# Optimization experiments

Measured on AMD Instinct MI355X. Metric: run time of the kernel, lower is better.

## Reference

```python
import jax, jax.numpy as jnp
import numpy as np

N_NODES = 100000


def gcn_conv(x, edge_index, W, b, n_nodes):
    # h = X W  (transform first, aggregate in the smaller hidden dim)
    h = x @ W
    src, dst = edge_index[0], edge_index[1]
    # add self-loops (GCNConv default, fill_value=1)
    loop = jnp.arange(n_nodes, dtype=src.dtype)
    src = jnp.concatenate([src, loop])
    dst = jnp.concatenate([dst, loop])
    w = jnp.ones(src.shape[0], dtype=x.dtype)
    # symmetric degree normalization: deg^{-1/2}[src] * w * deg^{-1/2}[dst]
    deg = jax.ops.segment_sum(w, dst, num_segments=n_nodes)
    dinv = jnp.where(deg > 0, jax.lax.rsqrt(deg), 0.0).astype(x.dtype)
    norm = dinv[src] * w * dinv[dst]
    # gather messages from src, scale, scatter-add into dst
    out = jax.ops.segment_sum(h[src] * norm[:, None], dst, num_segments=n_nodes)
    return out + b


def setup_inputs() -> dict:
    key = jax.random.key(0)
    k1, k2, k3, k4 = jax.random.split(key, 4)
    n, f, hid, c, e = N_NODES, 512, 64, 40, 1600000
    x = jax.random.normal(k1, (n, f), dtype=jnp.float32)
    edge_index = jax.random.randint(k2, (2, e), 0, n, dtype=jnp.int64)
    W1 = jax.random.normal(k3, (f, hid), dtype=jnp.float32) * (1.0 / np.sqrt(f))
    b1 = jnp.zeros((hid,), dtype=jnp.float32)
    W2 = jax.random.normal(k4, (hid, c), dtype=jnp.float32) * (1.0 / np.sqrt(hid))
    b2 = jnp.zeros((c,), dtype=jnp.float32)
    return {"x": x, "edge_index": edge_index, "W1": W1, "b1": b1, "W2": W2, "b2": b2}


def reference(x, edge_index, W1, b1, W2, b2):
    h = jax.nn.relu(gcn_conv(x, edge_index, W1, b1, N_NODES))
    # dropout is identity at inference (training=False)
    h = gcn_conv(h, edge_index, W2, b2, N_NODES)
    return jax.nn.log_softmax(h, axis=1)
```

## Files before the change

### kernel.cpp

```cpp
#include <hip/hip_runtime.h>
#include <hip/hip_bf16.h>
#include <hip/hip_fp16.h>
#include <cstddef>

#define N_NODES 100000
#define F_IN    512
#define HID     64
#define NCLS    40

#define CAP       64

#define NPART       8
#define PART_NODES  12500
#define PART_BLOCKS 256

using half8 = __attribute__((ext_vector_type(8))) _Float16;
using f32x4 = __attribute__((ext_vector_type(4))) float;

__global__ void zero_kernel(int* __restrict__ p, int n) {
    int i = blockIdx.x * blockDim.x + threadIdx.x;
    if (i < n) p[i] = 0;
}

__global__ __launch_bounds__(256) void scatter_part_kernel(const int* __restrict__ src,
                                                           const int* __restrict__ dst,
                                                           int* __restrict__ cur,
                                                           int* __restrict__ ebuf, int E) {
    const int p  = blockIdx.x & (NPART - 1);
    const int bi = blockIdx.x >> 3;
    const int nb = gridDim.x >> 3;
    const int lo = p * PART_NODES, hi = lo + PART_NODES;
    for (int e = bi * 256 + (int)threadIdx.x; e < E; e += nb * 256) {
        int d = dst[e];
        if (d >= lo && d < hi) {
            int pos = atomicAdd(&cur[d], 1);
            if (pos < CAP) ebuf[(size_t)d * CAP + pos] = src[e];
        }
    }
}

__global__ void make_dinv_kernel(const int* __restrict__ cur, float* __restrict__ dinv, int n) {
    int i = blockIdx.x * blockDim.x + threadIdx.x;
    if (i < n) dinv[i] = rsqrtf((float)(cur[i] + 1));
}

__global__ __launch_bounds__(256) void gemm1_mfma_kernel(const float* __restrict__ X,
                                                         const float* __restrict__ W,
                                                         __half* __restrict__ H, int M) {
    __shared__ _Float16 As[4][64][8];
    __shared__ _Float16 Bs[4][64][8];

    const int tid  = threadIdx.x;
    const int lane = tid & 63;
    const int w    = tid >> 6;
    const int l15  = lane & 15;
    const int kg   = lane >> 4;
    const int rowBase = blockIdx.x * 64;

    f32x4 acc[4] = {};

    for (int kt = 0; kt < F_IN; kt += 32) {
        #pragma unroll
        for (int p = 0; p < 2; ++p) {
            int idx = tid * 2 + p;
            int r = idx >> 3, k4 = idx & 7;
            int gr = rowBase + r; if (gr >= M) gr = M - 1;
            const float4 v = *reinterpret_cast<const float4*>(
                &X[(size_t)gr * F_IN + kt + k4 * 4]);
            _Float16* dstp = &As[k4 >> 1][r][(k4 & 1) * 4];
            dstp[0] = (_Float16)v.x; dstp[1] = (_Float16)v.y;
            dstp[2] = (_Float16)v.z; dstp[3] = (_Float16)v.w;
        }
        #pragma unroll
        for (int p = 0; p < 2; ++p) {
            int idx = tid * 2 + p;
            int k = idx >> 4, c4 = idx & 15;
            const float4 v = *reinterpret_cast<const float4*>(
                &W[(size_t)(kt + k) * HID + c4 * 4]);
            int kgg = k >> 3, j = k & 7;
            Bs[kgg][c4 * 4 + 0][j] = (_Float16)v.x;
            Bs[kgg][c4 * 4 + 1][j] = (_Float16)v.y;
            Bs[kgg][c4 * 4 + 2][j] = (_Float16)v.z;
            Bs[kgg][c4 * 4 + 3][j] = (_Float16)v.w;
        }
        __syncthreads();

        const half8 a = *reinterpret_cast<const half8*>(&As[kg][w * 16 + l15][0]);
        #pragma unroll
        for (int ct = 0; ct < 4; ++ct) {
            const half8 b = *reinterpret_cast<const half8*>(&Bs[kg][ct * 16 + l15][0]);
            acc[ct] = __builtin_amdgcn_mfma_f32_16x16x32_f16(a, b, acc[ct], 0, 0, 0);
        }
        __syncthreads();
    }

    #pragma unroll
    for (int ct = 0; ct < 4; ++ct) {
        #pragma unroll
        for (int r = 0; r < 4; ++r) {
            int grow = rowBase + w * 16 + kg * 4 + r;
            if (grow < M) H[(size_t)grow * HID + ct * 16 + l15] = __float2half(acc[ct][r]);
        }
    }
}

__global__ __launch_bounds__(256) void agg1_gemm2_kernel(const __half* __restrict__ h,
                                                         const int* __restrict__ ebuf,
                                                         const int* __restrict__ cur,
                                                         const float* __restrict__ dinv,
                                                         const float* __restrict__ b1,
                                                         const float* __restrict__ W2,
                                                         __half* __restrict__ h2) {
    __shared__ float W2s[HID * NCLS];
    __shared__ float zt[4][HID];

    const int tid  = threadIdx.x;
    const int lane = tid & 63;
    const int wv   = tid >> 6;
    const int n    = blockIdx.x * 4 + wv;

    for (int i = tid; i < HID * NCLS; i += 256) W2s[i] = W2[i];

    const float di = dinv[n];
    float acc = __half2float(h[(size_t)n * HID + lane]) * di * di;

    const int cnt = min(cur[n], CAP);
    const int* win = &ebuf[(size_t)n * CAP];

    int   s  = 0;
    float nm = 0.f;
    if (lane < cnt) {
        s  = win[lane];
        nm = dinv[s] * di;
    }
    int j = 0;
    for (; j + 4 <= cnt; j += 4) {
        int sa = __shfl(s, j);
        int sb = __shfl(s, j + 1);
        int sc = __shfl(s, j + 2);
        int sd = __shfl(s, j + 3);
        float na = __shfl(nm, j);
        float nb = __shfl(nm, j + 1);
        float nc = __shfl(nm, j + 2);
        float nd = __shfl(nm, j + 3);
        float va = __half2float(h[(size_t)sa * HID + lane]);
        float vb = __half2float(h[(size_t)sb * HID + lane]);
        float vc = __half2float(h[(size_t)sc * HID + lane]);
        float vd = __half2float(h[(size_t)sd * HID + lane]);
        acc = fmaf(va, na, acc);
        acc = fmaf(vb, nb, acc);
        acc = fmaf(vc, nc, acc);
        acc = fmaf(vd, nd, acc);
    }
    for (; j < cnt; ++j) {
        int sj = __shfl(s, j);
        float nj = __shfl(nm, j);
        acc = fmaf(__half2float(h[(size_t)sj * HID + lane]), nj, acc);
    }

    zt[wv][lane] = fmaxf(acc + b1[lane], 0.0f);
    __syncthreads();

    if (tid < 4 * NCLS) {
        int r = tid / NCLS, c = tid - r * NCLS;
        float sacc = 0.f;
        #pragma unroll
        for (int k = 0; k < HID; ++k)
            sacc = fmaf(zt[r][k], W2s[k * NCLS + c], sacc);
        h2[(size_t)(blockIdx.x * 4 + r) * 64 + c] = __float2half(sacc);
    }
}

__global__ __launch_bounds__(256) void agg2_lsm_kernel(const __half* __restrict__ h2,
                                                       const int* __restrict__ ebuf,
                                                       const int* __restrict__ cur,
                                                       const float* __restrict__ dinv,
                                                       const float* __restrict__ b2,
                                                       float* __restrict__ out, int M) {
    const int lane = threadIdx.x & 63;
    const int n = blockIdx.x * 4 + (threadIdx.x >> 6);
    if (n >= M) return;

    const bool act = (lane < NCLS);
    const float di = dinv[n];
    float acc = act ? __half2float(h2[(size_t)n * 64 + lane]) * di * di : 0.f;

    const int cnt = min(cur[n], CAP);
    const int* win = &ebuf[(size_t)n * CAP];

    int   s  = 0;
    float nm = 0.f;
    if (lane < cnt) {
        s  = win[lane];
        nm = dinv[s] * di;
    }
    int j = 0;
    for (; j + 4 <= cnt; j += 4) {
        int sa = __shfl(s, j);
        int sb = __shfl(s, j + 1);
        int sc = __shfl(s, j + 2);
        int sd = __shfl(s, j + 3);
        float na = __shfl(nm, j);
        float nb = __shfl(nm, j + 1);
        float nc = __shfl(nm, j + 2);
        float nd = __shfl(nm, j + 3);
        if (act) {
            float va = __half2float(h2[(size_t)sa * 64 + lane]);
            float vb = __half2float(h2[(size_t)sb * 64 + lane]);
            float vc = __half2float(h2[(size_t)sc * 64 + lane]);
            float vd = __half2float(h2[(size_t)sd * 64 + lane]);
            acc = fmaf(va, na, acc);
            acc = fmaf(vb, nb, acc);
            acc = fmaf(vc, nc, acc);
            acc = fmaf(vd, nd, acc);
        }
    }
    for (; j < cnt; ++j) {
        int sj = __shfl(s, j);
        float nj = __shfl(nm, j);
        if (act) acc = fmaf(__half2float(h2[(size_t)sj * 64 + lane]), nj, acc);
    }

    float logit = act ? (acc + b2[lane]) : -1e30f;
    float m = logit;
    #pragma unroll
    for (int o = 32; o >= 1; o >>= 1) m = fmaxf(m, __shfl_xor(m, o));
    float ex = act ? __expf(logit - m) : 0.f;
    float sm = ex;
    #pragma unroll
    for (int o = 32; o >= 1; o >>= 1) sm += __shfl_xor(sm, o);
    float res = logit - m - __logf(sm);

    if (act) out[(size_t)n * NCLS + lane] = res;
}

extern "C" void kernel_launch(void* const* d_in, const int* in_sizes, int n_in,
                              void* d_out, int out_size, void* d_ws, size_t ws_size,
                              hipStream_t stream) {
    const float* x  = (const float*)d_in[0];
    const int*   ei = (const int*)d_in[1];
    const float* W1 = (const float*)d_in[2];
    const float* b1 = (const float*)d_in[3];
    const float* W2 = (const float*)d_in[4];
    const float* b2 = (const float*)d_in[5];
    float* out = (float*)d_out;

    const int M = N_NODES;
    const int E = in_sizes[1] / 2;
    const int* src = ei;
    const int* dst = ei + E;

    char* ws = (char*)d_ws;
    int*    cur  = (int*)   (ws + 0);
    float*  dinv = (float*) (ws + 409600);
    int*    ebuf = (int*)   (ws + 819200);
    __half* h1   = (__half*)(ws + 26419200);
    __half* h2   = (__half*)(ws + 39219200);

    zero_kernel<<<(M + 255) / 256, 256, 0, stream>>>(cur, M);

    scatter_part_kernel<<<NPART * PART_BLOCKS, 256, 0, stream>>>(src, dst, cur, ebuf, E);
    make_dinv_kernel<<<(M + 255) / 256, 256, 0, stream>>>(cur, dinv, M);

    gemm1_mfma_kernel<<<(M + 63) / 64, 256, 0, stream>>>(x, W1, h1, M);

    agg1_gemm2_kernel<<<M / 4, 256, 0, stream>>>(h1, ebuf, cur, dinv, b1, W2, h2);

    agg2_lsm_kernel<<<(M + 3) / 4, 256, 0, stream>>>(h2, ebuf, cur, dinv, b2, out, M);
}
```

Baseline: 294.8 us.

## Merge edge scatter and first GEMM into one launch, compute dinv inline

Combines the partitioned edge-scatter kernel and the MFMA GEMM1 kernel into one grid, so scatter blocks and GEMM blocks run concurrently and the atomic-bound scatter overlaps the bandwidth-bound X@W1. The dinv array and its kernel are removed, and degree normalization is recomputed with rsqrtf from the clamped counts inside both aggregation kernels. This saves two launches and the dinv round trip, at the cost of extra rsqrt work and per-edge reads of cur[s] in place of dinv[s].

```diff
diff --git a/kernel.cpp b/kernel.cpp
--- a/kernel.cpp
+++ b/kernel.cpp
@@ -10,9 +10,10 @@
 
 #define CAP       64
 
-#define NPART       8
-#define PART_NODES  12500
-#define PART_BLOCKS 256
+#define NPART        8
+#define PART_NODES   12500
+#define SCAT_BLOCKS  2048
+#define GEMM1_BLOCKS 1563
 
 using half8 = __attribute__((ext_vector_type(8))) _Float16;
 using f32x4 = __attribute__((ext_vector_type(4))) float;
@@ -22,84 +23,79 @@
     if (i < n) p[i] = 0;
 }
 
-__global__ __launch_bounds__(256) void scatter_part_kernel(const int* __restrict__ src,
-                                                           const int* __restrict__ dst,
-                                                           int* __restrict__ cur,
-                                                           int* __restrict__ ebuf, int E) {
-    const int p  = blockIdx.x & (NPART - 1);
-    const int bi = blockIdx.x >> 3;
-    const int nb = gridDim.x >> 3;
-    const int lo = p * PART_NODES, hi = lo + PART_NODES;
-    for (int e = bi * 256 + (int)threadIdx.x; e < E; e += nb * 256) {
-        int d = dst[e];
-        if (d >= lo && d < hi) {
-            int pos = atomicAdd(&cur[d], 1);
-            if (pos < CAP) ebuf[(size_t)d * CAP + pos] = src[e];
-        }
-    }
-}
-
-__global__ void make_dinv_kernel(const int* __restrict__ cur, float* __restrict__ dinv, int n) {
-    int i = blockIdx.x * blockDim.x + threadIdx.x;
-    if (i < n) dinv[i] = rsqrtf((float)(cur[i] + 1));
-}
-
-__global__ __launch_bounds__(256) void gemm1_mfma_kernel(const float* __restrict__ X,
-                                                         const float* __restrict__ W,
-                                                         __half* __restrict__ H, int M) {
-    __shared__ _Float16 As[4][64][8];
-    __shared__ _Float16 Bs[4][64][8];
-
-    const int tid  = threadIdx.x;
-    const int lane = tid & 63;
-    const int w    = tid >> 6;
-    const int l15  = lane & 15;
-    const int kg   = lane >> 4;
-    const int rowBase = blockIdx.x * 64;
-
-    f32x4 acc[4] = {};
-
-    for (int kt = 0; kt < F_IN; kt += 32) {
-        #pragma unroll
-        for (int p = 0; p < 2; ++p) {
-            int idx = tid * 2 + p;
-            int r = idx >> 3, k4 = idx & 7;
-            int gr = rowBase + r; if (gr >= M) gr = M - 1;
-            const float4 v = *reinterpret_cast<const float4*>(
-                &X[(size_t)gr * F_IN + kt + k4 * 4]);
-            _Float16* dstp = &As[k4 >> 1][r][(k4 & 1) * 4];
-            dstp[0] = (_Float16)v.x; dstp[1] = (_Float16)v.y;
-            dstp[2] = (_Float16)v.z; dstp[3] = (_Float16)v.w;
-        }
-        #pragma unroll
-        for (int p = 0; p < 2; ++p) {
-            int idx = tid * 2 + p;
-            int k = idx >> 4, c4 = idx & 15;
-            const float4 v = *reinterpret_cast<const float4*>(
-                &W[(size_t)(kt + k) * HID + c4 * 4]);
-            int kgg = k >> 3, j = k & 7;
-            Bs[kgg][c4 * 4 + 0][j] = (_Float16)v.x;
-            Bs[kgg][c4 * 4 + 1][j] = (_Float16)v.y;
-            Bs[kgg][c4 * 4 + 2][j] = (_Float16)v.z;
-            Bs[kgg][c4 * 4 + 3][j] = (_Float16)v.w;
-        }
-        __syncthreads();
-
-        const half8 a = *reinterpret_cast<const half8*>(&As[kg][w * 16 + l15][0]);
+__global__ __launch_bounds__(256) void scatter_gemm1_kernel(const int* __restrict__ src,
+                                                            const int* __restrict__ dst,
+                                                            int* __restrict__ cur,
+                                                            int* __restrict__ ebuf, int E,
+                                                            const float* __restrict__ X,
+                                                            const float* __restrict__ W,
+                                                            __half* __restrict__ H, int M) {
+    if (blockIdx.x < SCAT_BLOCKS) {
+        const int p  = blockIdx.x & (NPART - 1);
+        const int bi = blockIdx.x >> 3;
+        const int lo = p * PART_NODES, hi = lo + PART_NODES;
+        for (int e = bi * 256 + (int)threadIdx.x; e < E; e += (SCAT_BLOCKS / NPART) * 256) {
+            int d = dst[e];
+            if (d >= lo && d < hi) {
+                int pos = atomicAdd(&cur[d], 1);
+                if (pos < CAP) ebuf[(size_t)d * CAP + pos] = src[e];
+            }
+        }
+    } else {
+        __shared__ _Float16 As[4][64][8];
+        __shared__ _Float16 Bs[4][64][8];
+
+        const int tid  = threadIdx.x;
+        const int lane = tid & 63;
+        const int w    = tid >> 6;
+        const int l15  = lane & 15;
+        const int kg   = lane >> 4;
+        const int rowBase = (blockIdx.x - SCAT_BLOCKS) * 64;
+
+        f32x4 acc[4] = {};
+
+        for (int kt = 0; kt < F_IN; kt += 32) {
+            #pragma unroll
+            for (int p = 0; p < 2; ++p) {
+                int idx = tid * 2 + p;
+                int r = idx >> 3, k4 = idx & 7;
+                int gr = rowBase + r; if (gr >= M) gr = M - 1;
+                const float4 v = *reinterpret_cast<const float4*>(
+                    &X[(size_t)gr * F_IN + kt + k4 * 4]);
+                _Float16* dstp = &As[k4 >> 1][r][(k4 & 1) * 4];
+                dstp[0] = (_Float16)v.x; dstp[1] = (_Float16)v.y;
+                dstp[2] = (_Float16)v.z; dstp[3] = (_Float16)v.w;
+            }
+            #pragma unroll
+            for (int p = 0; p < 2; ++p) {
+                int idx = tid * 2 + p;
+                int k = idx >> 4, c4 = idx & 15;
+                const float4 v = *reinterpret_cast<const float4*>(
+                    &W[(size_t)(kt + k) * HID + c4 * 4]);
+                int kgg = k >> 3, j = k & 7;
+                Bs[kgg][c4 * 4 + 0][j] = (_Float16)v.x;
+                Bs[kgg][c4 * 4 + 1][j] = (_Float16)v.y;
+                Bs[kgg][c4 * 4 + 2][j] = (_Float16)v.z;
+                Bs[kgg][c4 * 4 + 3][j] = (_Float16)v.w;
+            }
+            __syncthreads();
+
+            const half8 a = *reinterpret_cast<const half8*>(&As[kg][w * 16 + l15][0]);
+            #pragma unroll
+            for (int ct = 0; ct < 4; ++ct) {
+                const half8 b = *reinterpret_cast<const half8*>(&Bs[kg][ct * 16 + l15][0]);
+                acc[ct] = __builtin_amdgcn_mfma_f32_16x16x32_f16(a, b, acc[ct], 0, 0, 0);
+            }
+            __syncthreads();
+        }
+
         #pragma unroll
         for (int ct = 0; ct < 4; ++ct) {
-            const half8 b = *reinterpret_cast<const half8*>(&Bs[kg][ct * 16 + l15][0]);
-            acc[ct] = __builtin_amdgcn_mfma_f32_16x16x32_f16(a, b, acc[ct], 0, 0, 0);
-        }
-        __syncthreads();
-    }
-
-    #pragma unroll
-    for (int ct = 0; ct < 4; ++ct) {
-        #pragma unroll
-        for (int r = 0; r < 4; ++r) {
-            int grow = rowBase + w * 16 + kg * 4 + r;
-            if (grow < M) H[(size_t)grow * HID + ct * 16 + l15] = __float2half(acc[ct][r]);
+            #pragma unroll
+            for (int r = 0; r < 4; ++r) {
+                int grow = rowBase + w * 16 + kg * 4 + r;
+                if (grow < M) H[(size_t)grow * HID + ct * 16 + l15] = __float2half(acc[ct][r]);
+            }
         }
     }
 }
@@ -107,7 +103,6 @@
 __global__ __launch_bounds__(256) void agg1_gemm2_kernel(const __half* __restrict__ h,
                                                          const int* __restrict__ ebuf,
                                                          const int* __restrict__ cur,
-                                                         const float* __restrict__ dinv,
                                                          const float* __restrict__ b1,
                                                          const float* __restrict__ W2,
                                                          __half* __restrict__ h2) {
@@ -121,17 +116,17 @@
 
     for (int i = tid; i < HID * NCLS; i += 256) W2s[i] = W2[i];
 
-    const float di = dinv[n];
+    const int cnt = min(cur[n], CAP);
+    const float di = rsqrtf((float)(cnt + 1));
     float acc = __half2float(h[(size_t)n * HID + lane]) * di * di;
 
-    const int cnt = min(cur[n], CAP);
     const int* win = &ebuf[(size_t)n * CAP];
 
     int   s  = 0;
     float nm = 0.f;
     if (lane < cnt) {
         s  = win[lane];
-        nm = dinv[s] * di;
+        nm = rsqrtf((float)(min(cur[s], CAP) + 1)) * di;
     }
     int j = 0;
     for (; j + 4 <= cnt; j += 4) {
@@ -174,7 +169,6 @@
 __global__ __launch_bounds__(256) void agg2_lsm_kernel(const __half* __restrict__ h2,
                                                        const int* __restrict__ ebuf,
                                                        const int* __restrict__ cur,
-                                                       const float* __restrict__ dinv,
                                                        const float* __restrict__ b2,
                                                        float* __restrict__ out, int M) {
     const int lane = threadIdx.x & 63;
@@ -182,17 +176,17 @@
     if (n >= M) return;
 
     const bool act = (lane < NCLS);
-    const float di = dinv[n];
+    const int cnt = min(cur[n], CAP);
+    const float di = rsqrtf((float)(cnt + 1));
     float acc = act ? __half2float(h2[(size_t)n * 64 + lane]) * di * di : 0.f;
 
-    const int cnt = min(cur[n], CAP);
     const int* win = &ebuf[(size_t)n * CAP];
 
     int   s  = 0;
     float nm = 0.f;
     if (lane < cnt) {
         s  = win[lane];
-        nm = dinv[s] * di;
+        nm = rsqrtf((float)(min(cur[s], CAP) + 1)) * di;
     }
     int j = 0;
     for (; j + 4 <= cnt; j += 4) {
@@ -252,19 +246,16 @@
 
     char* ws = (char*)d_ws;
     int*    cur  = (int*)   (ws + 0);
-    float*  dinv = (float*) (ws + 409600);
-    int*    ebuf = (int*)   (ws + 819200);
-    __half* h1   = (__half*)(ws + 26419200);
-    __half* h2   = (__half*)(ws + 39219200);
+    int*    ebuf = (int*)   (ws + 409600);
+    __half* h1   = (__half*)(ws + 26009600);
+    __half* h2   = (__half*)(ws + 38809600);
 
     zero_kernel<<<(M + 255) / 256, 256, 0, stream>>>(cur, M);
 
-    scatter_part_kernel<<<NPART * PART_BLOCKS, 256, 0, stream>>>(src, dst, cur, ebuf, E);
-    make_dinv_kernel<<<(M + 255) / 256, 256, 0, stream>>>(cur, dinv, M);
-
-    gemm1_mfma_kernel<<<(M + 63) / 64, 256, 0, stream>>>(x, W1, h1, M);
-
-    agg1_gemm2_kernel<<<M / 4, 256, 0, stream>>>(h1, ebuf, cur, dinv, b1, W2, h2);
-
-    agg2_lsm_kernel<<<(M + 3) / 4, 256, 0, stream>>>(h2, ebuf, cur, dinv, b2, out, M);
-}
+    scatter_gemm1_kernel<<<SCAT_BLOCKS + GEMM1_BLOCKS, 256, 0, stream>>>(
+        src, dst, cur, ebuf, E, x, W1, h1, M);
+
+    agg1_gemm2_kernel<<<M / 4, 256, 0, stream>>>(h1, ebuf, cur, b1, W2, h2);
+
+    agg2_lsm_kernel<<<(M + 3) / 4, 256, 0, stream>>>(h2, ebuf, cur, b2, out, M);
+}
```

After: 294.6 us. About the same (-0.1%).
